# Performance work log

Hardware: AMD Instinct MI355X
Metric: run time of the kernel (lower is better)

Reference implementation:

```python
import jax, jax.numpy as jnp
import numpy as np

B, T, I, H, O = 256, 512, 64, 256, 1

def setup_inputs() -> dict:
    key = jax.random.key(0)
    ks = jax.random.split(key, 7)
    s_ih = 1.0 / np.sqrt(H)
    return {
        "x": jax.random.normal(ks[0], (B, T, I), dtype=jnp.float32),
        "W_ih": jax.random.uniform(ks[1], (H, I), jnp.float32, -s_ih, s_ih),
        "W_hh": jax.random.uniform(ks[2], (H, H), jnp.float32, -s_ih, s_ih),
        "b_ih": jax.random.uniform(ks[3], (H,), jnp.float32, -s_ih, s_ih),
        "b_hh": jax.random.uniform(ks[4], (H,), jnp.float32, -s_ih, s_ih),
        "fc_W": jax.random.uniform(ks[5], (O, H), jnp.float32, -s_ih, s_ih),
        "fc_b": jax.random.uniform(ks[6], (O,), jnp.float32, -s_ih, s_ih),
    }

def reference(x, W_ih, W_hh, b_ih, b_hh, fc_W, fc_b):
    # PyTorch RNN (tanh): h_t = tanh(x_t W_ih^T + b_ih + h_{t-1} W_hh^T + b_hh)
    # Precompute the input projection for all timesteps in one GEMM: [B,T,H]
    xW = jnp.einsum('bti,hi->bth', x, W_ih) + (b_ih + b_hh)
    xW_t = jnp.transpose(xW, (1, 0, 2))  # time-major [T,B,H] for scan
    h0 = jnp.zeros((x.shape[0], W_hh.shape[0]), dtype=x.dtype)

    def step(h, xw_t):
        h_new = jnp.tanh(xw_t + h @ W_hh.T)
        return h_new, None

    h_last, _ = jax.lax.scan(step, h0, xW_t)
    return h_last @ fc_W.T + fc_b  # [B,O]
```

## Files before the change

kernel.cpp:

```cpp
#include <hip/hip_runtime.h>


#define RNN_B 256
#define RNN_T 512
#define RNN_I 64
#define RNN_H 256
#define TILE_T 32
#define N_TILES (RNN_T / TILE_T)

__global__
__attribute__((amdgpu_flat_work_group_size(512, 512), amdgpu_waves_per_eu(2, 2)))
void rnn_fused_kernel(const float* __restrict__ x,
                      const float* __restrict__ W_ih,
                      const float* __restrict__ W_hh,
                      const float* __restrict__ b_ih,
                      const float* __restrict__ b_hh,
                      const float* __restrict__ fc_W,
                      const float* __restrict__ fc_b,
                      float* __restrict__ out)
{
    const int b   = blockIdx.x;
    const int tid = threadIdx.x;
    const int w   = tid >> 6;
    const int l   = tid & 63;
    const int g   = l >> 3;
    const int s   = l & 7;
    const int j0  = w * 32 + g * 4;

    __shared__ float hbuf[2][288];
    __shared__ float xt[TILE_T][RNN_I];
    __shared__ float red[8];

    float4 wh[4][8];
    float4 wi[4][2];
    #pragma unroll
    for (int jj = 0; jj < 4; ++jj) {
        const float4* src = reinterpret_cast<const float4*>(W_hh + (j0 + jj) * RNN_H + 32 * s);
        #pragma unroll
        for (int c = 0; c < 8; ++c) wh[jj][c] = src[c];
    }
    #pragma unroll
    for (int jj = 0; jj < 4; ++jj) {
        const float4* src = reinterpret_cast<const float4*>(W_ih + (j0 + jj) * RNN_I + 8 * s);
        #pragma unroll
        for (int c = 0; c < 2; ++c) wi[jj][c] = src[c];
    }

    const int   jjsel = ((s & 1) << 1) | ((s >> 1) & 1);
    const int   j_fin = j0 + jjsel;
    const int   jslot = j_fin + 4 * w;
    const float bias2 = b_ih[j_fin] + b_hh[j_fin];
    const float fcw   = fc_W[j_fin];

    if (tid < 288) hbuf[0][tid] = 0.0f;
    const float4* xs = reinterpret_cast<const float4*>(x + (size_t)b * RNN_T * RNN_I);
    float4 xreg = xs[tid];

    float hj = 0.0f;

#define RNN_STEP(CUR, NXT, TT)                                                  \
    {                                                                           \
        const float4* hs = reinterpret_cast<const float4*>(hbuf[CUR]) + 9 * s;  \
        const float4* xp = reinterpret_cast<const float4*>(&xt[TT][0]) + 2 * s; \
        float p0 = 0.f, p1 = 0.f, p2 = 0.f, p3 = 0.f;                           \
        _Pragma("unroll")                                                       \
        for (int c = 0; c < 8; ++c) {                                           \
            const float4 h4 = hs[c];       \
            p0 = fmaf(h4.x, wh[0][c].x, p0); p0 = fmaf(h4.y, wh[0][c].y, p0);   \
            p0 = fmaf(h4.z, wh[0][c].z, p0); p0 = fmaf(h4.w, wh[0][c].w, p0);   \
            p1 = fmaf(h4.x, wh[1][c].x, p1); p1 = fmaf(h4.y, wh[1][c].y, p1);   \
            p1 = fmaf(h4.z, wh[1][c].z, p1); p1 = fmaf(h4.w, wh[1][c].w, p1);   \
            p2 = fmaf(h4.x, wh[2][c].x, p2); p2 = fmaf(h4.y, wh[2][c].y, p2);   \
            p2 = fmaf(h4.z, wh[2][c].z, p2); p2 = fmaf(h4.w, wh[2][c].w, p2);   \
            p3 = fmaf(h4.x, wh[3][c].x, p3); p3 = fmaf(h4.y, wh[3][c].y, p3);   \
            p3 = fmaf(h4.z, wh[3][c].z, p3); p3 = fmaf(h4.w, wh[3][c].w, p3);   \
        }                                                                       \
        _Pragma("unroll")                                                       \
        for (int c = 0; c < 2; ++c) {                                           \
            const float4 x4 = xp[c];                                            \
            p0 = fmaf(x4.x, wi[0][c].x, p0); p0 = fmaf(x4.y, wi[0][c].y, p0);   \
            p0 = fmaf(x4.z, wi[0][c].z, p0); p0 = fmaf(x4.w, wi[0][c].w, p0);   \
            p1 = fmaf(x4.x, wi[1][c].x, p1); p1 = fmaf(x4.y, wi[1][c].y, p1);   \
            p1 = fmaf(x4.z, wi[1][c].z, p1); p1 = fmaf(x4.w, wi[1][c].w, p1);   \
            p2 = fmaf(x4.x, wi[2][c].x, p2); p2 = fmaf(x4.y, wi[2][c].y, p2);   \
            p2 = fmaf(x4.z, wi[2][c].z, p2); p2 = fmaf(x4.w, wi[2][c].w, p2);   \
            p3 = fmaf(x4.x, wi[3][c].x, p3); p3 = fmaf(x4.y, wi[3][c].y, p3);   \
            p3 = fmaf(x4.z, wi[3][c].z, p3); p3 = fmaf(x4.w, wi[3][c].w, p3);   \
        }                                                                       \
                       \
        const bool sb0 = (s & 1) != 0;                                          \
        const float g0 = sb0 ? p0 : p2, g1 = sb0 ? p1 : p3;      \
        const float k0 = sb0 ? p2 : p0, k1 = sb0 ? p3 : p1;       \
        const float r0 = k0 + __shfl_xor(g0, 1, 64);                            \
        const float r1 = k1 + __shfl_xor(g1, 1, 64);                            \
        const bool sb1 = (s & 2) != 0;                                          \
        const float g2 = sb1 ? r0 : r1;                                         \
        const float k2 = sb1 ? r1 : r0;                                         \
        const float u  = k2 + __shfl_xor(g2, 2, 64);                            \
        const float v  = u + __shfl_xor(u, 4, 64);          \
        const float z  = v + bias2;                                             \
        const float zc = fminf(fmaxf(z, -10.f), 10.f);                          \
        const float e  = exp2f(zc * 2.8853900817779268f);           \
        const float hn = (e - 1.f) * __builtin_amdgcn_rcpf(e + 1.f);            \
        hj = hn;                                                                \
        if (s < 4) hbuf[NXT][jslot] = hn;        \
        __syncthreads();                                                        \
    }

    for (int tile = 0; tile < N_TILES; ++tile) {
        reinterpret_cast<float4*>(xt)[tid] = xreg;
        if (tile + 1 < N_TILES) xreg = xs[(tile + 1) * 512 + tid];
        __syncthreads();

        for (int tt = 0; tt < TILE_T; tt += 2) {
            RNN_STEP(0, 1, tt)
            RNN_STEP(1, 0, tt + 1)
        }
    }
#undef RNN_STEP

    float term = (s < 4) ? hj * fcw : 0.0f;
    #pragma unroll
    for (int d = 1; d < 64; d <<= 1) term += __shfl_xor(term, d, 64);
    if (l == 0) red[w] = term;
    __syncthreads();
    if (tid == 0) {
        float sum = 0.f;
        #pragma unroll
        for (int ww = 0; ww < 8; ++ww) sum += red[ww];
        out[b] = sum + fc_b[0];
    }
}

extern "C" void kernel_launch(void* const* d_in, const int* in_sizes, int n_in,
                              void* d_out, int out_size, void* d_ws, size_t ws_size,
                              hipStream_t stream) {
    const float* x    = (const float*)d_in[0];
    const float* W_ih = (const float*)d_in[1];
    const float* W_hh = (const float*)d_in[2];
    const float* b_ih = (const float*)d_in[3];
    const float* b_hh = (const float*)d_in[4];
    const float* fc_W = (const float*)d_in[5];
    const float* fc_b = (const float*)d_in[6];
    float* out = (float*)d_out;

    rnn_fused_kernel<<<RNN_B, 512, 0, stream>>>(x, W_ih, W_hh, b_ih, b_hh, fc_W, fc_b, out);
}
```

Measured before the change: 319.5 us.

## Split RNN step across 1024 threads with packed FMA and DPP reductions

Doubles the block to 1024 threads so each lane covers 16 hidden inputs instead of 32, halving the per-step serial FMA chain. The dot products now use two-wide vector FMAs, which can map to packed fp32 FMA. The cross-lane reductions move from __shfl_xor to DPP and ds_swizzle, which avoid LDS round trips. The x tile doubles to 64 timesteps to fit the larger block. In exchange, each per-step __syncthreads now spans 16 waves, and the reduction gains a fourth level.

```diff
diff --git a/kernel.cpp b/kernel.cpp
--- a/kernel.cpp
+++ b/kernel.cpp
@@ -5,11 +5,24 @@
 #define RNN_T 512
 #define RNN_I 64
 #define RNN_H 256
-#define TILE_T 32
+#define TILE_T 64
 #define N_TILES (RNN_T / TILE_T)
 
+typedef float f32x2 __attribute__((ext_vector_type(2)));
+
+template <int CTRL>
+__device__ __forceinline__ float dppf(float v) {
+    return __builtin_bit_cast(float,
+        __builtin_amdgcn_update_dpp(0, __builtin_bit_cast(int, v),
+                                    CTRL, 0xF, 0xF, true));
+}
+__device__ __forceinline__ float swz_xor4(float v) {
+    return __builtin_bit_cast(float,
+        __builtin_amdgcn_ds_swizzle(__builtin_bit_cast(int, v), 0x101F));
+}
+
 __global__
-__attribute__((amdgpu_flat_work_group_size(512, 512), amdgpu_waves_per_eu(2, 2)))
+__attribute__((amdgpu_flat_work_group_size(1024, 1024), amdgpu_waves_per_eu(4, 4)))
 void rnn_fused_kernel(const float* __restrict__ x,
                       const float* __restrict__ W_ih,
                       const float* __restrict__ W_hh,
@@ -23,27 +36,28 @@
     const int tid = threadIdx.x;
     const int w   = tid >> 6;
     const int l   = tid & 63;
-    const int g   = l >> 3;
-    const int s   = l & 7;
-    const int j0  = w * 32 + g * 4;
+    const int g   = l >> 4;
+    const int s   = l & 15;
+    const int j0  = w * 16 + g * 4;
 
-    __shared__ float hbuf[2][288];
+    __shared__ float hbuf[2][320];
     __shared__ float xt[TILE_T][RNN_I];
-    __shared__ float red[8];
+    __shared__ float red[16];
 
-    float4 wh[4][8];
-    float4 wi[4][2];
+    f32x2 wh2[4][8];
+    f32x2 wi2[4][2];
     #pragma unroll
     for (int jj = 0; jj < 4; ++jj) {
-        const float4* src = reinterpret_cast<const float4*>(W_hh + (j0 + jj) * RNN_H + 32 * s);
+        const float4* src = reinterpret_cast<const float4*>(W_hh + (j0 + jj) * RNN_H + 16 * s);
         #pragma unroll
-        for (int c = 0; c < 8; ++c) wh[jj][c] = src[c];
-    }
-    #pragma unroll
-    for (int jj = 0; jj < 4; ++jj) {
-        const float4* src = reinterpret_cast<const float4*>(W_ih + (j0 + jj) * RNN_I + 8 * s);
-        #pragma unroll
-        for (int c = 0; c < 2; ++c) wi[jj][c] = src[c];
+        for (int c = 0; c < 4; ++c) {
+            const float4 v = src[c];
+            wh2[jj][2 * c + 0] = f32x2{v.x, v.y};
+            wh2[jj][2 * c + 1] = f32x2{v.z, v.w};
+        }
+        const float4 vi = *reinterpret_cast<const float4*>(W_ih + (j0 + jj) * RNN_I + 4 * s);
+        wi2[jj][0] = f32x2{vi.x, vi.y};
+        wi2[jj][1] = f32x2{vi.z, vi.w};
     }
 
     const int   jjsel = ((s & 1) << 1) | ((s >> 1) & 1);
@@ -52,64 +66,68 @@
     const float bias2 = b_ih[j_fin] + b_hh[j_fin];
     const float fcw   = fc_W[j_fin];
 
-    if (tid < 288) hbuf[0][tid] = 0.0f;
-    const float4* xs = reinterpret_cast<const float4*>(x + (size_t)b * RNN_T * RNN_I);
-    float4 xreg = xs[tid];
+    if (tid < 320) hbuf[0][tid] = 0.0f;
+    const float4* xs4 = reinterpret_cast<const float4*>(x + (size_t)b * RNN_T * RNN_I);
+    float4 xreg = xs4[tid];
 
     float hj = 0.0f;
 
 #define RNN_STEP(CUR, NXT, TT)                                                  \
     {                                                                           \
-        const float4* hs = reinterpret_cast<const float4*>(hbuf[CUR]) + 9 * s;  \
-        const float4* xp = reinterpret_cast<const float4*>(&xt[TT][0]) + 2 * s; \
-        float p0 = 0.f, p1 = 0.f, p2 = 0.f, p3 = 0.f;                           \
+        const float4* hs = reinterpret_cast<const float4*>(hbuf[CUR] + 20 * s); \
+        const float4  xv = *reinterpret_cast<const float4*>(&xt[TT][4 * s]);    \
+        f32x2 a0 = {0.f, 0.f}, a1 = {0.f, 0.f}, a2 = {0.f, 0.f}, a3 = {0.f, 0.f}; \
         _Pragma("unroll")                                                       \
-        for (int c = 0; c < 8; ++c) {                                           \
-            const float4 h4 = hs[c];       \
-            p0 = fmaf(h4.x, wh[0][c].x, p0); p0 = fmaf(h4.y, wh[0][c].y, p0);   \
-            p0 = fmaf(h4.z, wh[0][c].z, p0); p0 = fmaf(h4.w, wh[0][c].w, p0);   \
-            p1 = fmaf(h4.x, wh[1][c].x, p1); p1 = fmaf(h4.y, wh[1][c].y, p1);   \
-            p1 = fmaf(h4.z, wh[1][c].z, p1); p1 = fmaf(h4.w, wh[1][c].w, p1);   \
-            p2 = fmaf(h4.x, wh[2][c].x, p2); p2 = fmaf(h4.y, wh[2][c].y, p2);   \
-            p2 = fmaf(h4.z, wh[2][c].z, p2); p2 = fmaf(h4.w, wh[2][c].w, p2);   \
-            p3 = fmaf(h4.x, wh[3][c].x, p3); p3 = fmaf(h4.y, wh[3][c].y, p3);   \
-            p3 = fmaf(h4.z, wh[3][c].z, p3); p3 = fmaf(h4.w, wh[3][c].w, p3);   \
+        for (int c = 0; c < 4; ++c) {                                           \
+            const float4 h4 = hs[c];                                            \
+            const f32x2 hA = {h4.x, h4.y}, hB = {h4.z, h4.w};                   \
+            a0 = __builtin_elementwise_fma(hA, wh2[0][2 * c + 0], a0);          \
+            a0 = __builtin_elementwise_fma(hB, wh2[0][2 * c + 1], a0);          \
+            a1 = __builtin_elementwise_fma(hA, wh2[1][2 * c + 0], a1);          \
+            a1 = __builtin_elementwise_fma(hB, wh2[1][2 * c + 1], a1);          \
+            a2 = __builtin_elementwise_fma(hA, wh2[2][2 * c + 0], a2);          \
+            a2 = __builtin_elementwise_fma(hB, wh2[2][2 * c + 1], a2);          \
+            a3 = __builtin_elementwise_fma(hA, wh2[3][2 * c + 0], a3);          \
+            a3 = __builtin_elementwise_fma(hB, wh2[3][2 * c + 1], a3);          \
         }                                                                       \
-        _Pragma("unroll")                                                       \
-        for (int c = 0; c < 2; ++c) {                                           \
-            const float4 x4 = xp[c];                                            \
-            p0 = fmaf(x4.x, wi[0][c].x, p0); p0 = fmaf(x4.y, wi[0][c].y, p0);   \
-            p0 = fmaf(x4.z, wi[0][c].z, p0); p0 = fmaf(x4.w, wi[0][c].w, p0);   \
-            p1 = fmaf(x4.x, wi[1][c].x, p1); p1 = fmaf(x4.y, wi[1][c].y, p1);   \
-            p1 = fmaf(x4.z, wi[1][c].z, p1); p1 = fmaf(x4.w, wi[1][c].w, p1);   \
-            p2 = fmaf(x4.x, wi[2][c].x, p2); p2 = fmaf(x4.y, wi[2][c].y, p2);   \
-            p2 = fmaf(x4.z, wi[2][c].z, p2); p2 = fmaf(x4.w, wi[2][c].w, p2);   \
-            p3 = fmaf(x4.x, wi[3][c].x, p3); p3 = fmaf(x4.y, wi[3][c].y, p3);   \
-            p3 = fmaf(x4.z, wi[3][c].z, p3); p3 = fmaf(x4.w, wi[3][c].w, p3);   \
+        {                                                                       \
+            const f32x2 xA = {xv.x, xv.y}, xB = {xv.z, xv.w};                   \
+            a0 = __builtin_elementwise_fma(xA, wi2[0][0], a0);                  \
+            a0 = __builtin_elementwise_fma(xB, wi2[0][1], a0);                  \
+            a1 = __builtin_elementwise_fma(xA, wi2[1][0], a1);                  \
+            a1 = __builtin_elementwise_fma(xB, wi2[1][1], a1);                  \
+            a2 = __builtin_elementwise_fma(xA, wi2[2][0], a2);                  \
+            a2 = __builtin_elementwise_fma(xB, wi2[2][1], a2);                  \
+            a3 = __builtin_elementwise_fma(xA, wi2[3][0], a3);                  \
+            a3 = __builtin_elementwise_fma(xB, wi2[3][1], a3);                  \
         }                                                                       \
-                       \
+        float p0 = a0.x + a0.y, p1 = a1.x + a1.y;                               \
+        float p2 = a2.x + a2.y, p3 = a3.x + a3.y;                               \
+             \
+             \
         const bool sb0 = (s & 1) != 0;                                          \
-        const float g0 = sb0 ? p0 : p2, g1 = sb0 ? p1 : p3;      \
-        const float k0 = sb0 ? p2 : p0, k1 = sb0 ? p3 : p1;       \
-        const float r0 = k0 + __shfl_xor(g0, 1, 64);                            \
-        const float r1 = k1 + __shfl_xor(g1, 1, 64);                            \
+        const float g0 = sb0 ? p0 : p2, g1 = sb0 ? p1 : p3;                     \
+        const float k0 = sb0 ? p2 : p0, k1 = sb0 ? p3 : p1;                     \
+        const float r0 = k0 + dppf<0xB1>(g0);          \
+        const float r1 = k1 + dppf<0xB1>(g1);                                   \
         const bool sb1 = (s & 2) != 0;                                          \
         const float g2 = sb1 ? r0 : r1;                                         \
         const float k2 = sb1 ? r1 : r0;                                         \
-        const float u  = k2 + __shfl_xor(g2, 2, 64);                            \
-        const float v  = u + __shfl_xor(u, 4, 64);          \
-        const float z  = v + bias2;                                             \
+        float u = k2 + dppf<0x4E>(g2);                 \
+        u += swz_xor4(u);                                                       \
+        u += dppf<0x128>(u);                           \
+        const float z  = u + bias2;                                             \
         const float zc = fminf(fmaxf(z, -10.f), 10.f);                          \
         const float e  = exp2f(zc * 2.8853900817779268f);           \
         const float hn = (e - 1.f) * __builtin_amdgcn_rcpf(e + 1.f);            \
         hj = hn;                                                                \
-        if (s < 4) hbuf[NXT][jslot] = hn;        \
+        if (s < 4) hbuf[NXT][jslot] = hn;                                       \
         __syncthreads();                                                        \
     }
 
     for (int tile = 0; tile < N_TILES; ++tile) {
         reinterpret_cast<float4*>(xt)[tid] = xreg;
-        if (tile + 1 < N_TILES) xreg = xs[(tile + 1) * 512 + tid];
+        if (tile + 1 < N_TILES) xreg = xs4[(tile + 1) * 1024 + tid];
         __syncthreads();
 
         for (int tt = 0; tt < TILE_T; tt += 2) {
@@ -127,7 +145,7 @@
     if (tid == 0) {
         float sum = 0.f;
         #pragma unroll
-        for (int ww = 0; ww < 8; ++ww) sum += red[ww];
+        for (int ww = 0; ww < 16; ++ww) sum += red[ww];
         out[b] = sum + fc_b[0];
     }
 }
@@ -144,5 +162,5 @@
     const float* fc_b = (const float*)d_in[6];
     float* out = (float*)d_out;
 
-    rnn_fused_kernel<<<RNN_B, 512, 0, stream>>>(x, W_ih, W_hh, b_ih, b_hh, fc_W, fc_b, out);
+    rnn_fused_kernel<<<RNN_B, 1024, 0, stream>>>(x, W_ih, W_hh, b_ih, b_hh, fc_W, fc_b, out);
 }
```

Result: slower. 357.6 us (+11.9%).

## Halve block to 256 threads with eight hidden rows per thread

Applied to the files above, without the earlier changes.

Restructures the per-batch work split so each thread owns eight hidden units over a 32-wide slice instead of four, and the block shrinks from 512 to 256 threads (4 waves). Every lane now writes a unique h value and the reduction uses a three-level butterfly with no idle lanes. The input tile is halved to 16 timesteps to fit the smaller thread count. The aim is to cut barrier cost and duplicated reduction work per step. The cost is doubled register pressure (about 320 weight VGPRs per thread) and half the threads per CU, which relies on the wave-per-EU setting of 1.

```diff
diff --git a/kernel.cpp b/kernel.cpp
--- a/kernel.cpp
+++ b/kernel.cpp
@@ -5,11 +5,11 @@
 #define RNN_T 512
 #define RNN_I 64
 #define RNN_H 256
-#define TILE_T 32
+#define TILE_T 16
 #define N_TILES (RNN_T / TILE_T)
 
 __global__
-__attribute__((amdgpu_flat_work_group_size(512, 512), amdgpu_waves_per_eu(2, 2)))
+__attribute__((amdgpu_flat_work_group_size(256, 256), amdgpu_waves_per_eu(1, 1)))
 void rnn_fused_kernel(const float* __restrict__ x,
                       const float* __restrict__ W_ih,
                       const float* __restrict__ W_hh,
@@ -23,36 +23,33 @@
     const int tid = threadIdx.x;
     const int w   = tid >> 6;
     const int l   = tid & 63;
-    const int g   = l >> 3;
-    const int s   = l & 7;
-    const int j0  = w * 32 + g * 4;
+    const int r   = tid >> 3;
+    const int s   = tid & 7;
+    const int j0  = r * 8;
 
     __shared__ float hbuf[2][288];
     __shared__ float xt[TILE_T][RNN_I];
-    __shared__ float red[8];
+    __shared__ float red[4];
 
-    float4 wh[4][8];
-    float4 wi[4][2];
+    float4 wh[8][8];
+    float4 wi[8][2];
     #pragma unroll
-    for (int jj = 0; jj < 4; ++jj) {
+    for (int jj = 0; jj < 8; ++jj) {
         const float4* src = reinterpret_cast<const float4*>(W_hh + (j0 + jj) * RNN_H + 32 * s);
         #pragma unroll
         for (int c = 0; c < 8; ++c) wh[jj][c] = src[c];
-    }
-    #pragma unroll
-    for (int jj = 0; jj < 4; ++jj) {
-        const float4* src = reinterpret_cast<const float4*>(W_ih + (j0 + jj) * RNN_I + 8 * s);
-        #pragma unroll
-        for (int c = 0; c < 2; ++c) wi[jj][c] = src[c];
+        const float4* s2 = reinterpret_cast<const float4*>(W_ih + (j0 + jj) * RNN_I + 8 * s);
+        wi[jj][0] = s2[0];
+        wi[jj][1] = s2[1];
     }
 
-    const int   jjsel = ((s & 1) << 1) | ((s >> 1) & 1);
-    const int   j_fin = j0 + jjsel;
-    const int   jslot = j_fin + 4 * w;
+    const int   j_fin = j0 + s;
+    const int   jslot = j_fin + 4 * (j_fin >> 5);
     const float bias2 = b_ih[j_fin] + b_hh[j_fin];
     const float fcw   = fc_W[j_fin];
 
-    if (tid < 288) hbuf[0][tid] = 0.0f;
+    hbuf[0][tid] = 0.0f;
+    if (tid < 32) hbuf[0][256 + tid] = 0.0f;
     const float4* xs = reinterpret_cast<const float4*>(x + (size_t)b * RNN_T * RNN_I);
     float4 xreg = xs[tid];
 
@@ -62,54 +59,81 @@
     {                                                                           \
         const float4* hs = reinterpret_cast<const float4*>(hbuf[CUR]) + 9 * s;  \
         const float4* xp = reinterpret_cast<const float4*>(&xt[TT][0]) + 2 * s; \
-        float p0 = 0.f, p1 = 0.f, p2 = 0.f, p3 = 0.f;                           \
+        float a0=0.f,a1=0.f,a2=0.f,a3=0.f,a4=0.f,a5=0.f,a6=0.f,a7=0.f;          \
         _Pragma("unroll")                                                       \
         for (int c = 0; c < 8; ++c) {                                           \
             const float4 h4 = hs[c];       \
-            p0 = fmaf(h4.x, wh[0][c].x, p0); p0 = fmaf(h4.y, wh[0][c].y, p0);   \
-            p0 = fmaf(h4.z, wh[0][c].z, p0); p0 = fmaf(h4.w, wh[0][c].w, p0);   \
-            p1 = fmaf(h4.x, wh[1][c].x, p1); p1 = fmaf(h4.y, wh[1][c].y, p1);   \
-            p1 = fmaf(h4.z, wh[1][c].z, p1); p1 = fmaf(h4.w, wh[1][c].w, p1);   \
-            p2 = fmaf(h4.x, wh[2][c].x, p2); p2 = fmaf(h4.y, wh[2][c].y, p2);   \
-            p2 = fmaf(h4.z, wh[2][c].z, p2); p2 = fmaf(h4.w, wh[2][c].w, p2);   \
-            p3 = fmaf(h4.x, wh[3][c].x, p3); p3 = fmaf(h4.y, wh[3][c].y, p3);   \
-            p3 = fmaf(h4.z, wh[3][c].z, p3); p3 = fmaf(h4.w, wh[3][c].w, p3);   \
+            a0 = fmaf(h4.x, wh[0][c].x, a0); a1 = fmaf(h4.x, wh[1][c].x, a1);   \
+            a2 = fmaf(h4.x, wh[2][c].x, a2); a3 = fmaf(h4.x, wh[3][c].x, a3);   \
+            a4 = fmaf(h4.x, wh[4][c].x, a4); a5 = fmaf(h4.x, wh[5][c].x, a5);   \
+            a6 = fmaf(h4.x, wh[6][c].x, a6); a7 = fmaf(h4.x, wh[7][c].x, a7);   \
+            a0 = fmaf(h4.y, wh[0][c].y, a0); a1 = fmaf(h4.y, wh[1][c].y, a1);   \
+            a2 = fmaf(h4.y, wh[2][c].y, a2); a3 = fmaf(h4.y, wh[3][c].y, a3);   \
+            a4 = fmaf(h4.y, wh[4][c].y, a4); a5 = fmaf(h4.y, wh[5][c].y, a5);   \
+            a6 = fmaf(h4.y, wh[6][c].y, a6); a7 = fmaf(h4.y, wh[7][c].y, a7);   \
+            a0 = fmaf(h4.z, wh[0][c].z, a0); a1 = fmaf(h4.z, wh[1][c].z, a1);   \
+            a2 = fmaf(h4.z, wh[2][c].z, a2); a3 = fmaf(h4.z, wh[3][c].z, a3);   \
+            a4 = fmaf(h4.z, wh[4][c].z, a4); a5 = fmaf(h4.z, wh[5][c].z, a5);   \
+            a6 = fmaf(h4.z, wh[6][c].z, a6); a7 = fmaf(h4.z, wh[7][c].z, a7);   \
+            a0 = fmaf(h4.w, wh[0][c].w, a0); a1 = fmaf(h4.w, wh[1][c].w, a1);   \
+            a2 = fmaf(h4.w, wh[2][c].w, a2); a3 = fmaf(h4.w, wh[3][c].w, a3);   \
+            a4 = fmaf(h4.w, wh[4][c].w, a4); a5 = fmaf(h4.w, wh[5][c].w, a5);   \
+            a6 = fmaf(h4.w, wh[6][c].w, a6); a7 = fmaf(h4.w, wh[7][c].w, a7);   \
         }                                                                       \
         _Pragma("unroll")                                                       \
         for (int c = 0; c < 2; ++c) {                                           \
             const float4 x4 = xp[c];                                            \
-            p0 = fmaf(x4.x, wi[0][c].x, p0); p0 = fmaf(x4.y, wi[0][c].y, p0);   \
-            p0 = fmaf(x4.z, wi[0][c].z, p0); p0 = fmaf(x4.w, wi[0][c].w, p0);   \
-            p1 = fmaf(x4.x, wi[1][c].x, p1); p1 = fmaf(x4.y, wi[1][c].y, p1);   \
-            p1 = fmaf(x4.z, wi[1][c].z, p1); p1 = fmaf(x4.w, wi[1][c].w, p1);   \
-            p2 = fmaf(x4.x, wi[2][c].x, p2); p2 = fmaf(x4.y, wi[2][c].y, p2);   \
-            p2 = fmaf(x4.z, wi[2][c].z, p2); p2 = fmaf(x4.w, wi[2][c].w, p2);   \
-            p3 = fmaf(x4.x, wi[3][c].x, p3); p3 = fmaf(x4.y, wi[3][c].y, p3);   \
-            p3 = fmaf(x4.z, wi[3][c].z, p3); p3 = fmaf(x4.w, wi[3][c].w, p3);   \
+            a0 = fmaf(x4.x, wi[0][c].x, a0); a1 = fmaf(x4.x, wi[1][c].x, a1);   \
+            a2 = fmaf(x4.x, wi[2][c].x, a2); a3 = fmaf(x4.x, wi[3][c].x, a3);   \
+            a4 = fmaf(x4.x, wi[4][c].x, a4); a5 = fmaf(x4.x, wi[5][c].x, a5);   \
+            a6 = fmaf(x4.x, wi[6][c].x, a6); a7 = fmaf(x4.x, wi[7][c].x, a7);   \
+            a0 = fmaf(x4.y, wi[0][c].y, a0); a1 = fmaf(x4.y, wi[1][c].y, a1);   \
+            a2 = fmaf(x4.y, wi[2][c].y, a2); a3 = fmaf(x4.y, wi[3][c].y, a3);   \
+            a4 = fmaf(x4.y, wi[4][c].y, a4); a5 = fmaf(x4.y, wi[5][c].y, a5);   \
+            a6 = fmaf(x4.y, wi[6][c].y, a6); a7 = fmaf(x4.y, wi[7][c].y, a7);   \
+            a0 = fmaf(x4.z, wi[0][c].z, a0); a1 = fmaf(x4.z, wi[1][c].z, a1);   \
+            a2 = fmaf(x4.z, wi[2][c].z, a2); a3 = fmaf(x4.z, wi[3][c].z, a3);   \
+            a4 = fmaf(x4.z, wi[4][c].z, a4); a5 = fmaf(x4.z, wi[5][c].z, a5);   \
+            a6 = fmaf(x4.z, wi[6][c].z, a6); a7 = fmaf(x4.z, wi[7][c].z, a7);   \
+            a0 = fmaf(x4.w, wi[0][c].w, a0); a1 = fmaf(x4.w, wi[1][c].w, a1);   \
+            a2 = fmaf(x4.w, wi[2][c].w, a2); a3 = fmaf(x4.w, wi[3][c].w, a3);   \
+            a4 = fmaf(x4.w, wi[4][c].w, a4); a5 = fmaf(x4.w, wi[5][c].w, a5);   \
+            a6 = fmaf(x4.w, wi[6][c].w, a6); a7 = fmaf(x4.w, wi[7][c].w, a7);   \
         }                                                                       \
-                       \
-        const bool sb0 = (s & 1) != 0;                                          \
-        const float g0 = sb0 ? p0 : p2, g1 = sb0 ? p1 : p3;      \
-        const float k0 = sb0 ? p2 : p0, k1 = sb0 ? p3 : p1;       \
-        const float r0 = k0 + __shfl_xor(g0, 1, 64);                            \
-        const float r1 = k1 + __shfl_xor(g1, 1, 64);                            \
-        const bool sb1 = (s & 2) != 0;                                          \
-        const float g2 = sb1 ? r0 : r1;                                         \
-        const float k2 = sb1 ? r1 : r0;                                         \
-        const float u  = k2 + __shfl_xor(g2, 2, 64);                            \
-        const float v  = u + __shfl_xor(u, 4, 64);          \
+               \
+        const bool b0 = (s & 1) != 0;                                           \
+        const float k0 = b0 ? a1 : a0, g0 = b0 ? a0 : a1;                       \
+        const float k1 = b0 ? a3 : a2, g1 = b0 ? a2 : a3;                       \
+        const float k2 = b0 ? a5 : a4, g2 = b0 ? a4 : a5;                       \
+        const float k3 = b0 ? a7 : a6, g3 = b0 ? a6 : a7;                       \
+        const float q0 = k0 + __shfl_xor(g0, 1, 64);        \
+        const float q1 = k1 + __shfl_xor(g1, 1, 64);        \
+        const float q2 = k2 + __shfl_xor(g2, 1, 64);        \
+        const float q3 = k3 + __shfl_xor(g3, 1, 64);        \
+        const bool b1 = (s & 2) != 0;                                           \
+        const float m0 = b1 ? q1 : q0, n0 = b1 ? q0 : q1;                       \
+        const float m1 = b1 ? q3 : q2, n1 = b1 ? q2 : q3;                       \
+        const float u0 = m0 + __shfl_xor(n0, 2, 64);        \
+        const float u1 = m1 + __shfl_xor(n1, 2, 64);        \
+        const bool b2 = (s & 4) != 0;                                           \
+        const float mk = b2 ? u1 : u0, mg = b2 ? u0 : u1;                       \
+        const float v  = mk + __shfl_xor(mg, 4, 64);        \
         const float z  = v + bias2;                                             \
         const float zc = fminf(fmaxf(z, -10.f), 10.f);                          \
         const float e  = exp2f(zc * 2.8853900817779268f);           \
         const float hn = (e - 1.f) * __builtin_amdgcn_rcpf(e + 1.f);            \
         hj = hn;                                                                \
-        if (s < 4) hbuf[NXT][jslot] = hn;        \
+        hbuf[NXT][jslot] = hn;        \
         __syncthreads();                                                        \
     }
 
     for (int tile = 0; tile < N_TILES; ++tile) {
-        reinterpret_cast<float4*>(xt)[tid] = xreg;
-        if (tile + 1 < N_TILES) xreg = xs[(tile + 1) * 512 + tid];
+        {
+            const int st = tid >> 4;
+            const int of = (tid & 15) << 2;
+            *reinterpret_cast<float4*>(&xt[st][of]) = xreg;
+        }
+        if (tile + 1 < N_TILES) xreg = xs[(tile + 1) * 256 + tid];
         __syncthreads();
 
         for (int tt = 0; tt < TILE_T; tt += 2) {
@@ -119,17 +143,12 @@
     }
 #undef RNN_STEP
 
-    float term = (s < 4) ? hj * fcw : 0.0f;
+    float term = hj * fcw;
     #pragma unroll
     for (int d = 1; d < 64; d <<= 1) term += __shfl_xor(term, d, 64);
     if (l == 0) red[w] = term;
     __syncthreads();
-    if (tid == 0) {
-        float sum = 0.f;
-        #pragma unroll
-        for (int ww = 0; ww < 8; ++ww) sum += red[ww];
-        out[b] = sum + fc_b[0];
-    }
+    if (tid == 0) out[b] = red[0] + red[1] + red[2] + red[3] + fc_b[0];
 }
 
 extern "C" void kernel_launch(void* const* d_in, const int* in_sizes, int n_in,
@@ -144,5 +163,5 @@
     const float* fc_b = (const float*)d_in[6];
     float* out = (float*)d_out;
 
-    rnn_fused_kernel<<<RNN_B, 512, 0, stream>>>(x, W_ih, W_hh, b_ih, b_hh, fc_W, fc_b, out);
+    rnn_fused_kernel<<<RNN_B, 256, 0, stream>>>(x, W_ih, W_hh, b_ih, b_hh, fc_W, fc_b, out);
 }
```

Result: slower. 998.0 us (+212.4%).

## Hand-write the recurrent step loop in inline GCN assembly with packed FMAs

Applied to the files above, without the earlier changes.

Replaces the compiler-generated time-step loop with a single inline-assembly block. Weights stay pinned in fixed VGPRs, the dot products use v_pk_fma_f32, and the LDS reads are issued early with staged lgkmcnt waits so FMAs overlap the loads. The lane reduction uses ds_bpermute with cndmask swaps. Lanes with s>=4 now write to a dummy slot instead of branching. This aims to cut per-step latency on the serial recurrence, but it is fragile: hardcoded registers, a manual s_nop hazard, and a clobber list the compiler must respect.

```diff
diff --git a/kernel.cpp b/kernel.cpp
--- a/kernel.cpp
+++ b/kernel.cpp
@@ -1,12 +1,143 @@
 #include <hip/hip_runtime.h>
+#include <stdint.h>
 
 
 #define RNN_B 256
 #define RNN_T 512
 #define RNN_I 64
 #define RNN_H 256
-#define TILE_T 32
-#define N_TILES (RNN_T / TILE_T)
+
+#define STEP(RD, WR) \
+  "ds_read_b128 v[0:3], "   RD " offset:0\n\t" \
+  "ds_read_b128 v[4:7], "   RD " offset:16\n\t" \
+  "ds_read_b128 v[8:11], "  RD " offset:32\n\t" \
+  "ds_read_b128 v[12:15], " RD " offset:48\n\t" \
+  "ds_read_b128 v[16:19], " RD " offset:64\n\t" \
+  "ds_read_b128 v[20:23], " RD " offset:80\n\t" \
+  "ds_read_b128 v[24:27], " RD " offset:96\n\t" \
+  "ds_read_b128 v[28:31], " RD " offset:112\n\t" \
+  "ds_read_b128 v[32:35], v55 offset:0\n\t" \
+  "ds_read_b128 v[48:51], v55 offset:16\n\t" \
+  "v_add_u32 v55, 0x100, v55\n\t" \
+  "s_waitcnt lgkmcnt(6)\n\t" \
+  "v_pk_mul_f32 v[36:37], v[0:1], v[64:65]\n\t" \
+  "v_pk_mul_f32 v[38:39], v[0:1], v[96:97]\n\t" \
+  "v_pk_mul_f32 v[40:41], v[0:1], v[128:129]\n\t" \
+  "v_pk_mul_f32 v[42:43], v[0:1], v[160:161]\n\t" \
+  "v_pk_fma_f32 v[36:37], v[2:3], v[66:67], v[36:37]\n\t" \
+  "v_pk_fma_f32 v[38:39], v[2:3], v[98:99], v[38:39]\n\t" \
+  "v_pk_fma_f32 v[40:41], v[2:3], v[130:131], v[40:41]\n\t" \
+  "v_pk_fma_f32 v[42:43], v[2:3], v[162:163], v[42:43]\n\t" \
+  "v_pk_fma_f32 v[36:37], v[4:5], v[68:69], v[36:37]\n\t" \
+  "v_pk_fma_f32 v[38:39], v[4:5], v[100:101], v[38:39]\n\t" \
+  "v_pk_fma_f32 v[40:41], v[4:5], v[132:133], v[40:41]\n\t" \
+  "v_pk_fma_f32 v[42:43], v[4:5], v[164:165], v[42:43]\n\t" \
+  "v_pk_fma_f32 v[36:37], v[6:7], v[70:71], v[36:37]\n\t" \
+  "v_pk_fma_f32 v[38:39], v[6:7], v[102:103], v[38:39]\n\t" \
+  "v_pk_fma_f32 v[40:41], v[6:7], v[134:135], v[40:41]\n\t" \
+  "v_pk_fma_f32 v[42:43], v[6:7], v[166:167], v[42:43]\n\t" \
+  "v_pk_fma_f32 v[36:37], v[8:9], v[72:73], v[36:37]\n\t" \
+  "v_pk_fma_f32 v[38:39], v[8:9], v[104:105], v[38:39]\n\t" \
+  "v_pk_fma_f32 v[40:41], v[8:9], v[136:137], v[40:41]\n\t" \
+  "v_pk_fma_f32 v[42:43], v[8:9], v[168:169], v[42:43]\n\t" \
+  "v_pk_fma_f32 v[36:37], v[10:11], v[74:75], v[36:37]\n\t" \
+  "v_pk_fma_f32 v[38:39], v[10:11], v[106:107], v[38:39]\n\t" \
+  "v_pk_fma_f32 v[40:41], v[10:11], v[138:139], v[40:41]\n\t" \
+  "v_pk_fma_f32 v[42:43], v[10:11], v[170:171], v[42:43]\n\t" \
+  "v_pk_fma_f32 v[36:37], v[12:13], v[76:77], v[36:37]\n\t" \
+  "v_pk_fma_f32 v[38:39], v[12:13], v[108:109], v[38:39]\n\t" \
+  "v_pk_fma_f32 v[40:41], v[12:13], v[140:141], v[40:41]\n\t" \
+  "v_pk_fma_f32 v[42:43], v[12:13], v[172:173], v[42:43]\n\t" \
+  "v_pk_fma_f32 v[36:37], v[14:15], v[78:79], v[36:37]\n\t" \
+  "v_pk_fma_f32 v[38:39], v[14:15], v[110:111], v[38:39]\n\t" \
+  "v_pk_fma_f32 v[40:41], v[14:15], v[142:143], v[40:41]\n\t" \
+  "v_pk_fma_f32 v[42:43], v[14:15], v[174:175], v[42:43]\n\t" \
+  "s_waitcnt lgkmcnt(2)\n\t" \
+  "v_pk_fma_f32 v[36:37], v[16:17], v[80:81], v[36:37]\n\t" \
+  "v_pk_fma_f32 v[38:39], v[16:17], v[112:113], v[38:39]\n\t" \
+  "v_pk_fma_f32 v[40:41], v[16:17], v[144:145], v[40:41]\n\t" \
+  "v_pk_fma_f32 v[42:43], v[16:17], v[176:177], v[42:43]\n\t" \
+  "v_pk_fma_f32 v[36:37], v[18:19], v[82:83], v[36:37]\n\t" \
+  "v_pk_fma_f32 v[38:39], v[18:19], v[114:115], v[38:39]\n\t" \
+  "v_pk_fma_f32 v[40:41], v[18:19], v[146:147], v[40:41]\n\t" \
+  "v_pk_fma_f32 v[42:43], v[18:19], v[178:179], v[42:43]\n\t" \
+  "v_pk_fma_f32 v[36:37], v[20:21], v[84:85], v[36:37]\n\t" \
+  "v_pk_fma_f32 v[38:39], v[20:21], v[116:117], v[38:39]\n\t" \
+  "v_pk_fma_f32 v[40:41], v[20:21], v[148:149], v[40:41]\n\t" \
+  "v_pk_fma_f32 v[42:43], v[20:21], v[180:181], v[42:43]\n\t" \
+  "v_pk_fma_f32 v[36:37], v[22:23], v[86:87], v[36:37]\n\t" \
+  "v_pk_fma_f32 v[38:39], v[22:23], v[118:119], v[38:39]\n\t" \
+  "v_pk_fma_f32 v[40:41], v[22:23], v[150:151], v[40:41]\n\t" \
+  "v_pk_fma_f32 v[42:43], v[22:23], v[182:183], v[42:43]\n\t" \
+  "v_pk_fma_f32 v[36:37], v[24:25], v[88:89], v[36:37]\n\t" \
+  "v_pk_fma_f32 v[38:39], v[24:25], v[120:121], v[38:39]\n\t" \
+  "v_pk_fma_f32 v[40:41], v[24:25], v[152:153], v[40:41]\n\t" \
+  "v_pk_fma_f32 v[42:43], v[24:25], v[184:185], v[42:43]\n\t" \
+  "v_pk_fma_f32 v[36:37], v[26:27], v[90:91], v[36:37]\n\t" \
+  "v_pk_fma_f32 v[38:39], v[26:27], v[122:123], v[38:39]\n\t" \
+  "v_pk_fma_f32 v[40:41], v[26:27], v[154:155], v[40:41]\n\t" \
+  "v_pk_fma_f32 v[42:43], v[26:27], v[186:187], v[42:43]\n\t" \
+  "v_pk_fma_f32 v[36:37], v[28:29], v[92:93], v[36:37]\n\t" \
+  "v_pk_fma_f32 v[38:39], v[28:29], v[124:125], v[38:39]\n\t" \
+  "v_pk_fma_f32 v[40:41], v[28:29], v[156:157], v[40:41]\n\t" \
+  "v_pk_fma_f32 v[42:43], v[28:29], v[188:189], v[42:43]\n\t" \
+  "v_pk_fma_f32 v[36:37], v[30:31], v[94:95], v[36:37]\n\t" \
+  "v_pk_fma_f32 v[38:39], v[30:31], v[126:127], v[38:39]\n\t" \
+  "v_pk_fma_f32 v[40:41], v[30:31], v[158:159], v[40:41]\n\t" \
+  "v_pk_fma_f32 v[42:43], v[30:31], v[190:191], v[42:43]\n\t" \
+  "s_waitcnt lgkmcnt(0)\n\t" \
+  "v_pk_fma_f32 v[36:37], v[32:33], v[192:193], v[36:37]\n\t" \
+  "v_pk_fma_f32 v[38:39], v[32:33], v[200:201], v[38:39]\n\t" \
+  "v_pk_fma_f32 v[40:41], v[32:33], v[208:209], v[40:41]\n\t" \
+  "v_pk_fma_f32 v[42:43], v[32:33], v[216:217], v[42:43]\n\t" \
+  "v_pk_fma_f32 v[36:37], v[34:35], v[194:195], v[36:37]\n\t" \
+  "v_pk_fma_f32 v[38:39], v[34:35], v[202:203], v[38:39]\n\t" \
+  "v_pk_fma_f32 v[40:41], v[34:35], v[210:211], v[40:41]\n\t" \
+  "v_pk_fma_f32 v[42:43], v[34:35], v[218:219], v[42:43]\n\t" \
+  "v_pk_fma_f32 v[36:37], v[48:49], v[196:197], v[36:37]\n\t" \
+  "v_pk_fma_f32 v[38:39], v[48:49], v[204:205], v[38:39]\n\t" \
+  "v_pk_fma_f32 v[40:41], v[48:49], v[212:213], v[40:41]\n\t" \
+  "v_pk_fma_f32 v[42:43], v[48:49], v[220:221], v[42:43]\n\t" \
+  "v_pk_fma_f32 v[36:37], v[50:51], v[198:199], v[36:37]\n\t" \
+  "v_pk_fma_f32 v[38:39], v[50:51], v[206:207], v[38:39]\n\t" \
+  "v_pk_fma_f32 v[40:41], v[50:51], v[214:215], v[40:41]\n\t" \
+  "v_pk_fma_f32 v[42:43], v[50:51], v[222:223], v[42:43]\n\t" \
+  "v_add_f32 v44, v36, v37\n\t" \
+  "v_add_f32 v45, v38, v39\n\t" \
+  "v_add_f32 v46, v40, v41\n\t" \
+  "v_add_f32 v47, v42, v43\n\t" \
+  "v_cndmask_b32 v52, v46, v44, %[m1]\n\t" \
+  "v_cndmask_b32 v44, v44, v46, %[m1]\n\t" \
+  "v_cndmask_b32 v53, v47, v45, %[m1]\n\t" \
+  "v_cndmask_b32 v45, v45, v47, %[m1]\n\t" \
+  "ds_bpermute_b32 v52, %[bp1], v52\n\t" \
+  "ds_bpermute_b32 v53, %[bp1], v53\n\t" \
+  "s_waitcnt lgkmcnt(0)\n\t" \
+  "v_add_f32 v44, v44, v52\n\t" \
+  "v_add_f32 v45, v45, v53\n\t" \
+  "v_cndmask_b32 v52, v45, v44, %[m2]\n\t" \
+  "v_cndmask_b32 v44, v44, v45, %[m2]\n\t" \
+  "ds_bpermute_b32 v52, %[bp2], v52\n\t" \
+  "s_waitcnt lgkmcnt(0)\n\t" \
+  "v_add_f32 v44, v44, v52\n\t" \
+  "ds_bpermute_b32 v52, %[bp4], v44\n\t" \
+  "s_waitcnt lgkmcnt(0)\n\t" \
+  "v_add_f32 v44, v44, v52\n\t" \
+  "v_add_f32 v44, %[bias], v44\n\t" \
+  "v_max_f32 v44, %[klo], v44\n\t" \
+  "v_min_f32 v44, %[khi], v44\n\t" \
+  "v_mul_f32 v44, %[km], v44\n\t" \
+  "v_exp_f32 v53, v44\n\t" \
+  "s_nop 1\n\t" \
+  "v_subrev_f32 v54, 1.0, v53\n\t" \
+  "v_add_f32 v53, 1.0, v53\n\t" \
+  "v_rcp_f32 v53, v53\n\t" \
+  "s_nop 1\n\t" \
+  "v_mul_f32 v54, v54, v53\n\t" \
+  "v_mov_b32 %[hj], v54\n\t" \
+  "ds_write_b32 " WR ", v54\n\t" \
+  "s_waitcnt lgkmcnt(0)\n\t" \
+  "s_barrier\n\t"
 
 __global__
 __attribute__((amdgpu_flat_work_group_size(512, 512), amdgpu_waves_per_eu(2, 2)))
@@ -27,97 +158,150 @@
     const int s   = l & 7;
     const int j0  = w * 32 + g * 4;
 
-    __shared__ float hbuf[2][288];
-    __shared__ float xt[TILE_T][RNN_I];
+    __shared__ float hbuf[2][320];
+    __shared__ float xt[32][RNN_I];
     __shared__ float red[8];
-
-    float4 wh[4][8];
-    float4 wi[4][2];
-    #pragma unroll
-    for (int jj = 0; jj < 4; ++jj) {
-        const float4* src = reinterpret_cast<const float4*>(W_hh + (j0 + jj) * RNN_H + 32 * s);
-        #pragma unroll
-        for (int c = 0; c < 8; ++c) wh[jj][c] = src[c];
-    }
-    #pragma unroll
-    for (int jj = 0; jj < 4; ++jj) {
-        const float4* src = reinterpret_cast<const float4*>(W_ih + (j0 + jj) * RNN_I + 8 * s);
-        #pragma unroll
-        for (int c = 0; c < 2; ++c) wi[jj][c] = src[c];
-    }
 
     const int   jjsel = ((s & 1) << 1) | ((s >> 1) & 1);
     const int   j_fin = j0 + jjsel;
     const int   jslot = j_fin + 4 * w;
+    const int   wslot = (s < 4) ? jslot : (288 + (l & 31));
     const float bias2 = b_ih[j_fin] + b_hh[j_fin];
     const float fcw   = fc_W[j_fin];
 
-    if (tid < 288) hbuf[0][tid] = 0.0f;
-    const float4* xs = reinterpret_cast<const float4*>(x + (size_t)b * RNN_T * RNN_I);
-    float4 xreg = xs[tid];
+    const uint32_t hb   = (uint32_t)(uintptr_t)&hbuf[0][0];
+    const uint32_t xtb  = (uint32_t)(uintptr_t)&xt[0][0];
+    const uint32_t hrd0 = hb + 144u * (uint32_t)s;
+    const uint32_t hrd1 = hb + 1280u + 144u * (uint32_t)s;
+    const uint32_t hwr0 = hb + 4u * (uint32_t)wslot;
+    const uint32_t hwr1 = hb + 1280u + 4u * (uint32_t)wslot;
+    const uint32_t xst  = xtb + 16u * (uint32_t)tid;
+    const uint32_t xrd0 = xtb + 32u * (uint32_t)s;
+
+    const uint32_t bp1 = (uint32_t)((l ^ 1) << 2);
+    const uint32_t bp2 = (uint32_t)((l ^ 2) << 2);
+    const uint32_t bp4 = (uint32_t)((l ^ 4) << 2);
+    const unsigned long long m1 = __ballot(s & 1);
+    const unsigned long long m2 = __ballot(s & 2);
+
+    const float* whp = W_hh + (size_t)j0 * RNN_H + 32 * s;
+    const float* wip = W_ih + (size_t)j0 * RNN_I + 8 * s;
+    const float* xgp = x + (size_t)b * RNN_T * RNN_I + 4 * tid;
+    const uint32_t whlo = (uint32_t)(uintptr_t)whp, whhi = (uint32_t)((uintptr_t)whp >> 32);
+    const uint32_t wilo = (uint32_t)(uintptr_t)wip, wihi = (uint32_t)((uintptr_t)wip >> 32);
+    const uint32_t xglo = (uint32_t)(uintptr_t)xgp, xghi = (uint32_t)((uintptr_t)xgp >> 32);
+
+    if (tid < 320) hbuf[0][tid] = 0.0f;
+    __syncthreads();
 
     float hj = 0.0f;
-
-#define RNN_STEP(CUR, NXT, TT)                                                  \
-    {                                                                           \
-        const float4* hs = reinterpret_cast<const float4*>(hbuf[CUR]) + 9 * s;  \
-        const float4* xp = reinterpret_cast<const float4*>(&xt[TT][0]) + 2 * s; \
-        float p0 = 0.f, p1 = 0.f, p2 = 0.f, p3 = 0.f;                           \
-        _Pragma("unroll")                                                       \
-        for (int c = 0; c < 8; ++c) {                                           \
-            const float4 h4 = hs[c];       \
-            p0 = fmaf(h4.x, wh[0][c].x, p0); p0 = fmaf(h4.y, wh[0][c].y, p0);   \
-            p0 = fmaf(h4.z, wh[0][c].z, p0); p0 = fmaf(h4.w, wh[0][c].w, p0);   \
-            p1 = fmaf(h4.x, wh[1][c].x, p1); p1 = fmaf(h4.y, wh[1][c].y, p1);   \
-            p1 = fmaf(h4.z, wh[1][c].z, p1); p1 = fmaf(h4.w, wh[1][c].w, p1);   \
-            p2 = fmaf(h4.x, wh[2][c].x, p2); p2 = fmaf(h4.y, wh[2][c].y, p2);   \
-            p2 = fmaf(h4.z, wh[2][c].z, p2); p2 = fmaf(h4.w, wh[2][c].w, p2);   \
-            p3 = fmaf(h4.x, wh[3][c].x, p3); p3 = fmaf(h4.y, wh[3][c].y, p3);   \
-            p3 = fmaf(h4.z, wh[3][c].z, p3); p3 = fmaf(h4.w, wh[3][c].w, p3);   \
-        }                                                                       \
-        _Pragma("unroll")                                                       \
-        for (int c = 0; c < 2; ++c) {                                           \
-            const float4 x4 = xp[c];                                            \
-            p0 = fmaf(x4.x, wi[0][c].x, p0); p0 = fmaf(x4.y, wi[0][c].y, p0);   \
-            p0 = fmaf(x4.z, wi[0][c].z, p0); p0 = fmaf(x4.w, wi[0][c].w, p0);   \
-            p1 = fmaf(x4.x, wi[1][c].x, p1); p1 = fmaf(x4.y, wi[1][c].y, p1);   \
-            p1 = fmaf(x4.z, wi[1][c].z, p1); p1 = fmaf(x4.w, wi[1][c].w, p1);   \
-            p2 = fmaf(x4.x, wi[2][c].x, p2); p2 = fmaf(x4.y, wi[2][c].y, p2);   \
-            p2 = fmaf(x4.z, wi[2][c].z, p2); p2 = fmaf(x4.w, wi[2][c].w, p2);   \
-            p3 = fmaf(x4.x, wi[3][c].x, p3); p3 = fmaf(x4.y, wi[3][c].y, p3);   \
-            p3 = fmaf(x4.z, wi[3][c].z, p3); p3 = fmaf(x4.w, wi[3][c].w, p3);   \
-        }                                                                       \
-                       \
-        const bool sb0 = (s & 1) != 0;                                          \
-        const float g0 = sb0 ? p0 : p2, g1 = sb0 ? p1 : p3;      \
-        const float k0 = sb0 ? p2 : p0, k1 = sb0 ? p3 : p1;       \
-        const float r0 = k0 + __shfl_xor(g0, 1, 64);                            \
-        const float r1 = k1 + __shfl_xor(g1, 1, 64);                            \
-        const bool sb1 = (s & 2) != 0;                                          \
-        const float g2 = sb1 ? r0 : r1;                                         \
-        const float k2 = sb1 ? r1 : r0;                                         \
-        const float u  = k2 + __shfl_xor(g2, 2, 64);                            \
-        const float v  = u + __shfl_xor(u, 4, 64);          \
-        const float z  = v + bias2;                                             \
-        const float zc = fminf(fmaxf(z, -10.f), 10.f);                          \
-        const float e  = exp2f(zc * 2.8853900817779268f);           \
-        const float hn = (e - 1.f) * __builtin_amdgcn_rcpf(e + 1.f);            \
-        hj = hn;                                                                \
-        if (s < 4) hbuf[NXT][jslot] = hn;        \
-        __syncthreads();                                                        \
-    }
-
-    for (int tile = 0; tile < N_TILES; ++tile) {
-        reinterpret_cast<float4*>(xt)[tid] = xreg;
-        if (tile + 1 < N_TILES) xreg = xs[(tile + 1) * 512 + tid];
-        __syncthreads();
-
-        for (int tt = 0; tt < TILE_T; tt += 2) {
-            RNN_STEP(0, 1, tt)
-            RNN_STEP(1, 0, tt + 1)
-        }
-    }
-#undef RNN_STEP
+    int cntt, cnts, sadv;
+    const float khi = 10.0f, klo = -10.0f, km = 2.8853900817779268f;
+
+    asm volatile(
+        "v_mov_b32 v56, %[whlo]\n\t"
+        "v_mov_b32 v57, %[whhi]\n\t"
+        "global_load_dwordx4 v[64:67],   v[56:57], off\n\t"
+        "global_load_dwordx4 v[68:71],   v[56:57], off offset:16\n\t"
+        "global_load_dwordx4 v[72:75],   v[56:57], off offset:32\n\t"
+        "global_load_dwordx4 v[76:79],   v[56:57], off offset:48\n\t"
+        "global_load_dwordx4 v[80:83],   v[56:57], off offset:64\n\t"
+        "global_load_dwordx4 v[84:87],   v[56:57], off offset:80\n\t"
+        "global_load_dwordx4 v[88:91],   v[56:57], off offset:96\n\t"
+        "global_load_dwordx4 v[92:95],   v[56:57], off offset:112\n\t"
+        "global_load_dwordx4 v[96:99],   v[56:57], off offset:1024\n\t"
+        "global_load_dwordx4 v[100:103], v[56:57], off offset:1040\n\t"
+        "global_load_dwordx4 v[104:107], v[56:57], off offset:1056\n\t"
+        "global_load_dwordx4 v[108:111], v[56:57], off offset:1072\n\t"
+        "global_load_dwordx4 v[112:115], v[56:57], off offset:1088\n\t"
+        "global_load_dwordx4 v[116:119], v[56:57], off offset:1104\n\t"
+        "global_load_dwordx4 v[120:123], v[56:57], off offset:1120\n\t"
+        "global_load_dwordx4 v[124:127], v[56:57], off offset:1136\n\t"
+        "global_load_dwordx4 v[128:131], v[56:57], off offset:2048\n\t"
+        "global_load_dwordx4 v[132:135], v[56:57], off offset:2064\n\t"
+        "global_load_dwordx4 v[136:139], v[56:57], off offset:2080\n\t"
+        "global_load_dwordx4 v[140:143], v[56:57], off offset:2096\n\t"
+        "global_load_dwordx4 v[144:147], v[56:57], off offset:2112\n\t"
+        "global_load_dwordx4 v[148:151], v[56:57], off offset:2128\n\t"
+        "global_load_dwordx4 v[152:155], v[56:57], off offset:2144\n\t"
+        "global_load_dwordx4 v[156:159], v[56:57], off offset:2160\n\t"
+        "global_load_dwordx4 v[160:163], v[56:57], off offset:3072\n\t"
+        "global_load_dwordx4 v[164:167], v[56:57], off offset:3088\n\t"
+        "global_load_dwordx4 v[168:171], v[56:57], off offset:3104\n\t"
+        "global_load_dwordx4 v[172:175], v[56:57], off offset:3120\n\t"
+        "global_load_dwordx4 v[176:179], v[56:57], off offset:3136\n\t"
+        "global_load_dwordx4 v[180:183], v[56:57], off offset:3152\n\t"
+        "global_load_dwordx4 v[184:187], v[56:57], off offset:3168\n\t"
+        "global_load_dwordx4 v[188:191], v[56:57], off offset:3184\n\t"
+        "v_mov_b32 v56, %[wilo]\n\t"
+        "v_mov_b32 v57, %[wihi]\n\t"
+        "global_load_dwordx4 v[192:195], v[56:57], off\n\t"
+        "global_load_dwordx4 v[196:199], v[56:57], off offset:16\n\t"
+        "global_load_dwordx4 v[200:203], v[56:57], off offset:256\n\t"
+        "global_load_dwordx4 v[204:207], v[56:57], off offset:272\n\t"
+        "global_load_dwordx4 v[208:211], v[56:57], off offset:512\n\t"
+        "global_load_dwordx4 v[212:215], v[56:57], off offset:528\n\t"
+        "global_load_dwordx4 v[216:219], v[56:57], off offset:768\n\t"
+        "global_load_dwordx4 v[220:223], v[56:57], off offset:784\n\t"
+        "v_mov_b32 v58, %[xglo]\n\t"
+        "v_mov_b32 v59, %[xghi]\n\t"
+        "global_load_dwordx4 v[60:63], v[58:59], off\n\t"
+        "v_add_co_u32 v58, vcc, 0x2000, v58\n\t"
+        "v_addc_co_u32 v59, vcc, 0, v59, vcc\n\t"
+        "s_mov_b32 %[cntt], 16\n\t"
+        "LTILE%=:\n\t"
+        "s_waitcnt vmcnt(0)\n\t"
+        "ds_write_b128 %[xst], v[60:63]\n\t"
+        "global_load_dwordx4 v[60:63], v[58:59], off\n\t"
+        "s_cmp_lg_u32 %[cntt], 2\n\t"
+        "s_cselect_b32 %[sadv], 0x2000, 0\n\t"
+        "v_add_co_u32 v58, vcc, %[sadv], v58\n\t"
+        "v_addc_co_u32 v59, vcc, 0, v59, vcc\n\t"
+        "v_mov_b32 v55, %[xrd0]\n\t"
+        "s_waitcnt lgkmcnt(0)\n\t"
+        "s_barrier\n\t"
+        "s_mov_b32 %[cnts], 16\n\t"
+        "LSTEP%=:\n\t"
+        STEP("%[hrd0]", "%[hwr1]")
+        STEP("%[hrd1]", "%[hwr0]")
+        "s_sub_u32 %[cnts], %[cnts], 1\n\t"
+        "s_cmp_lg_u32 %[cnts], 0\n\t"
+        "s_cbranch_scc1 LSTEP%=\n\t"
+        "s_sub_u32 %[cntt], %[cntt], 1\n\t"
+        "s_cmp_lg_u32 %[cntt], 0\n\t"
+        "s_cbranch_scc1 LTILE%=\n\t"
+        "s_waitcnt vmcnt(0)\n\t"
+        : [hj] "+v"(hj), [cntt] "=&s"(cntt), [cnts] "=&s"(cnts), [sadv] "=&s"(sadv)
+        : [whlo] "v"(whlo), [whhi] "v"(whhi), [wilo] "v"(wilo), [wihi] "v"(wihi),
+          [xglo] "v"(xglo), [xghi] "v"(xghi), [xst] "v"(xst), [xrd0] "v"(xrd0),
+          [hrd0] "v"(hrd0), [hrd1] "v"(hrd1), [hwr0] "v"(hwr0), [hwr1] "v"(hwr1),
+          [bp1] "v"(bp1), [bp2] "v"(bp2), [bp4] "v"(bp4), [bias] "v"(bias2),
+          [m1] "s"(m1), [m2] "s"(m2),
+          [khi] "s"(khi), [klo] "s"(klo), [km] "s"(km)
+        : "memory", "vcc", "scc",
+          "v0","v1","v2","v3","v4","v5","v6","v7","v8","v9",
+          "v10","v11","v12","v13","v14","v15","v16","v17","v18","v19",
+          "v20","v21","v22","v23","v24","v25","v26","v27","v28","v29",
+          "v30","v31","v32","v33","v34","v35","v36","v37","v38","v39",
+          "v40","v41","v42","v43","v44","v45","v46","v47","v48","v49",
+          "v50","v51","v52","v53","v54","v55","v56","v57","v58","v59",
+          "v60","v61","v62","v63","v64","v65","v66","v67","v68","v69",
+          "v70","v71","v72","v73","v74","v75","v76","v77","v78","v79",
+          "v80","v81","v82","v83","v84","v85","v86","v87","v88","v89",
+          "v90","v91","v92","v93","v94","v95","v96","v97","v98","v99",
+          "v100","v101","v102","v103","v104","v105","v106","v107","v108","v109",
+          "v110","v111","v112","v113","v114","v115","v116","v117","v118","v119",
+          "v120","v121","v122","v123","v124","v125","v126","v127","v128","v129",
+          "v130","v131","v132","v133","v134","v135","v136","v137","v138","v139",
+          "v140","v141","v142","v143","v144","v145","v146","v147","v148","v149",
+          "v150","v151","v152","v153","v154","v155","v156","v157","v158","v159",
+          "v160","v161","v162","v163","v164","v165","v166","v167","v168","v169",
+          "v170","v171","v172","v173","v174","v175","v176","v177","v178","v179",
+          "v180","v181","v182","v183","v184","v185","v186","v187","v188","v189",
+          "v190","v191","v192","v193","v194","v195","v196","v197","v198","v199",
+          "v200","v201","v202","v203","v204","v205","v206","v207","v208","v209",
+          "v210","v211","v212","v213","v214","v215","v216","v217","v218","v219",
+          "v220","v221","v222","v223");
 
     float term = (s < 4) ? hj * fcw : 0.0f;
     #pragma unroll
```

New measurement: 342.8 us. 1.07x slower.
